# Kernel optimization log

Measured on AMD Instinct MI355X. Metric: run time of the kernel, lower is better.

Reference implementation:

```python
import jax, jax.numpy as jnp
import numpy as np
import math

N_HEAD = 16
DEG = 2
EPS = 1e-7


def setup_inputs() -> dict:
    key = jax.random.key(0)
    k1, k2 = jax.random.split(key)
    B, T, C = 2, 2048, 1024
    x = jax.random.normal(k1, (B, T, C), dtype=jnp.float32)
    W = jax.random.normal(k2, (3 * C + N_HEAD, C), dtype=jnp.float32) * (1.0 / math.sqrt(C))
    return {"x": x, "W": W}


def reference(x, W):
    # JacobAttentionLayer.forward with attention_kernel='powerref' (AttentionReference,
    # deg=2, scale=1/sqrt(hs), eps=1e-7, log-space power softmax, gating=True).
    B, T, C = x.shape
    nh = N_HEAD
    hs = C // nh
    scale = 1.0 / math.sqrt(hs)

    qkvgr = jnp.einsum('btc,oc->bto', x, W)  # [B,T,3C+nh]
    q, k, v = (qkvgr[..., :C], qkvgr[..., C:2 * C], qkvgr[..., 2 * C:3 * C])
    log_g = jax.nn.log_sigmoid(qkvgr[..., 3 * C:].astype(jnp.float32))  # [B,T,nh]
    log_G = jnp.cumsum(log_g, axis=1).transpose(0, 2, 1)  # [B,nh,T]

    def heads(a):  # [B,T,C] -> [B,nh,T,hs]
        return a.reshape(B, T, nh, hs).transpose(0, 2, 1, 3)

    Q, K, V = heads(q), heads(k), heads(v)

    S = jnp.einsum('bhtd,bhsd->bhts', Q, K)  # [B,nh,T,T]
    # log-space power attention: deg*log(|S|+eps) + log(scale) + gating
    Tm = DEG * jnp.log(jnp.abs(S) + EPS) + jnp.log(jnp.float32(scale))
    Z = Tm + log_G[..., :, None] - log_G[..., None, :]
    mask = jnp.tril(jnp.ones((T, T), dtype=bool))
    Z = jnp.where(mask, Z, -jnp.inf)
    Z_rowmax = jax.lax.stop_gradient(jnp.max(Z, axis=-1, keepdims=True))
    P = jnp.exp(Z - Z_rowmax)  # deg even -> no sign correction

    norm = jnp.sum(P, axis=-1)  # [B,nh,T]
    O = jnp.einsum('bhts,bhsd->bhtd', P, V)
    y = O / norm[..., None]
    return y.transpose(0, 2, 1, 3).reshape(B, T, C)
```

## Files before the change

### kernel.cpp

```cpp
#include <hip/hip_runtime.h>
#include <math.h>

typedef __attribute__((ext_vector_type(4))) float f32x4;
typedef __attribute__((ext_vector_type(8))) short short8;

#define NEG_INF (-__builtin_inff())

__device__ __forceinline__ unsigned short f2bf(float f) {
    union { float f; unsigned u; } v; v.f = f;
    unsigned r = v.u + 0x7FFFu + ((v.u >> 16) & 1u);
    return (unsigned short)(r >> 16);
}
__device__ __forceinline__ float bf2f(unsigned short h) {
    union { unsigned u; float f; } v; v.u = ((unsigned)h) << 16;
    return v.f;
}

__device__ __forceinline__ f32x4 mfma_bf16(short8 a, short8 b, f32x4 c) {
    return __builtin_amdgcn_mfma_f32_16x16x32_bf16(a, b, c, 0, 0, 0);
}

__device__ __forceinline__ void gload_lds16(const unsigned short* g, unsigned short* l) {
    __builtin_amdgcn_global_load_lds(
        (const __attribute__((address_space(1))) void*)g,
        (__attribute__((address_space(3))) void*)l, 16, 0, 0);
}

__global__ void split_kernel(const float* __restrict__ in,
                             unsigned short* __restrict__ hi,
                             unsigned short* __restrict__ lo, int n4)
{
    int i = blockIdx.x * 256 + threadIdx.x;
    if (i >= n4) return;
    float4 v = ((const float4*)in)[i];
    ushort4 h, l;
    h.x = f2bf(v.x); l.x = f2bf(v.x - bf2f(h.x));
    h.y = f2bf(v.y); l.y = f2bf(v.y - bf2f(h.y));
    h.z = f2bf(v.z); l.z = f2bf(v.z - bf2f(h.z));
    h.w = f2bf(v.w); l.w = f2bf(v.w - bf2f(h.w));
    ((ushort4*)hi)[i] = h;
    ((ushort4*)lo)[i] = l;
}

__global__ __launch_bounds__(256, 2)
void gemm_proj(const unsigned short* __restrict__ xh, const unsigned short* __restrict__ xl,
               const unsigned short* __restrict__ wh, const unsigned short* __restrict__ wl,
               unsigned short* __restrict__ Qh, unsigned short* __restrict__ Ql,
               unsigned short* __restrict__ Kh, unsigned short* __restrict__ Kl,
               unsigned short* __restrict__ Vtg, float* __restrict__ gbuf)
{
    __shared__ __align__(16) unsigned short Ah[2][128][32];
    __shared__ __align__(16) unsigned short Al[2][128][32];
    __shared__ __align__(16) unsigned short Bh[2][128][32];
    __shared__ __align__(16) unsigned short Bl[2][128][32];

    const int mt = blockIdx.x & 31;
    const int nt = blockIdx.x >> 5;
    const int m0 = mt * 128, n0 = nt * 128;
    const int tid = threadIdx.x;
    const int w = tid >> 6, l = tid & 63;
    const int wm = w >> 1, wn = w & 1;
    const int lr = l & 15, lq = l >> 4;
    const int xs = (lr >> 1) & 3;
    const bool needLo = (nt < 16) || (nt == 24);

    f32x4 acc[4][4];
#pragma unroll
    for (int i = 0; i < 4; ++i)
#pragma unroll
        for (int j = 0; j < 4; ++j) acc[i][j] = (f32x4){0.f, 0.f, 0.f, 0.f};

    const int srow = tid >> 2;
    const int sp = tid & 3;

    auto STAGE = [&](int bsel, int k0) {
#pragma unroll
        for (int p = 0; p < 2; ++p) {
            int r = srow + p * 64;
            int sc = (sp ^ ((r >> 1) & 3)) * 8;
            int o = n0 + r;
            int oc = o < 3088 ? o : 3087;
            gload_lds16(&xh[(size_t)(m0 + r) * 1024 + k0 + sc], &Ah[bsel][r][sp * 8]);
            gload_lds16(&wh[(size_t)oc * 1024 + k0 + sc],       &Bh[bsel][r][sp * 8]);
            if (needLo) {
                gload_lds16(&xl[(size_t)(m0 + r) * 1024 + k0 + sc], &Al[bsel][r][sp * 8]);
                gload_lds16(&wl[(size_t)oc * 1024 + k0 + sc],       &Bl[bsel][r][sp * 8]);
            }
        }
    };

    STAGE(0, 0);
    __asm__ volatile("s_waitcnt vmcnt(0)" ::: "memory");
    __syncthreads();

    int cur = 0;
    for (int k0 = 0; k0 < 1024; k0 += 32) {
        if (k0 + 32 < 1024) STAGE(cur ^ 1, k0 + 32);

        short8 ah[4], bh4[4], al4[4], bl4[4];
#pragma unroll
        for (int i = 0; i < 4; ++i) {
            ah[i]  = *(const short8*)&Ah[cur][wm * 64 + i * 16 + lr][(lq ^ xs) * 8];
            bh4[i] = *(const short8*)&Bh[cur][wn * 64 + i * 16 + lr][(lq ^ xs) * 8];
        }
        if (needLo) {
#pragma unroll
            for (int i = 0; i < 4; ++i) {
                al4[i] = *(const short8*)&Al[cur][wm * 64 + i * 16 + lr][(lq ^ xs) * 8];
                bl4[i] = *(const short8*)&Bl[cur][wn * 64 + i * 16 + lr][(lq ^ xs) * 8];
            }
        }
#pragma unroll
        for (int i = 0; i < 4; ++i)
#pragma unroll
            for (int j = 0; j < 4; ++j) {
                acc[i][j] = mfma_bf16(ah[i], bh4[j], acc[i][j]);
                if (needLo) {
                    acc[i][j] = mfma_bf16(ah[i], bl4[j], acc[i][j]);
                    acc[i][j] = mfma_bf16(al4[i], bh4[j], acc[i][j]);
                }
            }

        __asm__ volatile("s_waitcnt vmcnt(0)" ::: "memory");
        __syncthreads();
        cur ^= 1;
    }

#pragma unroll
    for (int i = 0; i < 4; ++i) {
        int nrow0 = m0 + wm * 64 + i * 16 + lq * 4;
        int b = nrow0 >> 11;
        int tbase = nrow0 & 2047;
#pragma unroll
        for (int j = 0; j < 4; ++j) {
            int o = n0 + wn * 64 + j * 16 + lr;
            if (o < 1024) {
                int h = o >> 6, d = o & 63;
                size_t base = ((size_t)(b * 16 + h) * 2048 + tbase) * 64 + d;
#pragma unroll
                for (int r = 0; r < 4; ++r) {
                    float v = acc[i][j][r];
                    unsigned short hi_ = f2bf(v);
                    unsigned short lo_ = f2bf(v - bf2f(hi_));
                    Qh[base + (size_t)r * 64] = hi_;
                    Ql[base + (size_t)r * 64] = lo_;
                }
            } else if (o < 2048) {
                int oo = o - 1024;
                int h = oo >> 6, d = oo & 63;
                size_t base = ((size_t)(b * 16 + h) * 2048 + tbase) * 64 + d;
#pragma unroll
                for (int r = 0; r < 4; ++r) {
                    float v = acc[i][j][r];
                    unsigned short hi_ = f2bf(v);
                    unsigned short lo_ = f2bf(v - bf2f(hi_));
                    Kh[base + (size_t)r * 64] = hi_;
                    Kl[base + (size_t)r * 64] = lo_;
                }
            } else if (o < 3072) {
                int oo = o - 2048;
                int h = oo >> 6, d = oo & 63;
                size_t base = ((size_t)(b * 16 + h) * 64 + d) * 2048 + tbase;
                ushort4 pk;
                pk.x = f2bf(acc[i][j][0]);
                pk.y = f2bf(acc[i][j][1]);
                pk.z = f2bf(acc[i][j][2]);
                pk.w = f2bf(acc[i][j][3]);
                *(ushort4*)&Vtg[base] = pk;
            } else if (o < 3088) {
                int og = o - 3072;
#pragma unroll
                for (int r = 0; r < 4; ++r)
                    gbuf[(size_t)(nrow0 + r) * 16 + og] = acc[i][j][r];
            }
        }
    }
}

__global__ void gate_scan(const float* __restrict__ g, float* __restrict__ lg)
{
    const int bh = blockIdx.x;
    const int b = bh >> 4, h = bh & 15;
    const int tid = threadIdx.x;
    __shared__ float part[256];

    float vals[8];
    float run = 0.f;
#pragma unroll
    for (int j = 0; j < 8; ++j) {
        int t = tid * 8 + j;
        float x = g[(size_t)(b * 2048 + t) * 16 + h];
        float ls = fminf(x, 0.f) - log1pf(__expf(-fabsf(x)));
        run += ls * 1.4426950408889634f;
        vals[j] = run;
    }
    part[tid] = run;
    __syncthreads();
    for (int ofs = 1; ofs < 256; ofs <<= 1) {
        float add = (tid >= ofs) ? part[tid - ofs] : 0.f;
        __syncthreads();
        part[tid] += add;
        __syncthreads();
    }
    float excl = part[tid] - run;
#pragma unroll
    for (int j = 0; j < 8; ++j)
        lg[(size_t)bh * 2048 + tid * 8 + j] = excl + vals[j];
}

__global__ __launch_bounds__(256, 2)
void attn_fwd(const unsigned short* __restrict__ Qh, const unsigned short* __restrict__ Ql,
              const unsigned short* __restrict__ Kh, const unsigned short* __restrict__ Kl,
              const unsigned short* __restrict__ Vtg, const float* __restrict__ lg,
              float* __restrict__ out)
{
    __shared__ __align__(16) unsigned short kh[2][64][64];
    __shared__ __align__(16) unsigned short kl[2][64][64];
    __shared__ __align__(16) unsigned short vs[2][64][64];
    __shared__ __align__(16) unsigned short pl[4][16][64];

    const int bid = blockIdx.x;
    const int qi = (bid & 7) | ((bid >> 8) << 3);
    const int bh = (bid >> 3) & 31;
    const int tid = threadIdx.x;
    const int w = tid >> 6, l = tid & 63;
    const int lr = l & 15, lq = l >> 4;
    const int xk = lr & 7;
    const int q0 = qi * 64;
    const int myrow0 = q0 + w * 16;

    const size_t qoff = ((size_t)bh * 2048 + myrow0 + lr) * 64;
    short8 qh8[2], ql8[2];
    qh8[0] = *(const short8*)&Qh[qoff + lq * 8];
    qh8[1] = *(const short8*)&Qh[qoff + 32 + lq * 8];
    ql8[0] = *(const short8*)&Ql[qoff + lq * 8];
    ql8[1] = *(const short8*)&Ql[qoff + 32 + lq * 8];

    float gq2[4];
#pragma unroll
    for (int r = 0; r < 4; ++r)
        gq2[r] = lg[(size_t)bh * 2048 + myrow0 + lq * 4 + r] - 3.0f;

    float M_[4]  = {0.f, 0.f, 0.f, 0.f};
    float ls_[4] = {0.f, 0.f, 0.f, 0.f};
    f32x4 o4[4];
#pragma unroll
    for (int i = 0; i < 4; ++i) o4[i] = (f32x4){0.f, 0.f, 0.f, 0.f};

    const int srow = tid >> 3;
    const int schunk = tid & 7;

    const unsigned short* Kh_b = Kh + (size_t)bh * 2048 * 64;
    const unsigned short* Kl_b = Kl + (size_t)bh * 2048 * 64;
    const unsigned short* Vt_b = Vtg + (size_t)bh * 64 * 2048;

    auto STAGE = [&](int bsel, int kv0) {
#pragma unroll
        for (int p = 0; p < 2; ++p) {
            int r = srow + p * 32;
            int sc = (schunk ^ (r & 7)) * 8;
            gload_lds16(&Kh_b[(size_t)(kv0 + r) * 64 + sc], &kh[bsel][r][schunk * 8]);
            gload_lds16(&Kl_b[(size_t)(kv0 + r) * 64 + sc], &kl[bsel][r][schunk * 8]);
            gload_lds16(&Vt_b[(size_t)r * 2048 + kv0 + sc], &vs[bsel][r][schunk * 8]);
        }
    };

    STAGE(0, 0);
    __asm__ volatile("s_waitcnt vmcnt(0)" ::: "memory");
    __syncthreads();

    int cur = 0;
    for (int kv0 = 0; kv0 <= q0; kv0 += 64) {
        if (kv0 + 64 <= q0) STAGE(cur ^ 1, kv0 + 64);

        float gsl[4];
#pragma unroll
        for (int js = 0; js < 4; ++js)
            gsl[js] = lg[(size_t)bh * 2048 + kv0 + js * 16 + lr];

        f32x4 sa[4];
#pragma unroll
        for (int js = 0; js < 4; ++js) sa[js] = (f32x4){0.f, 0.f, 0.f, 0.f};
#pragma unroll
        for (int js = 0; js < 4; ++js)
#pragma unroll
            for (int ks = 0; ks < 2; ++ks) {
                short8 kb  = *(const short8*)&kh[cur][js * 16 + lr][((ks * 4 + lq) ^ xk) << 3];
                short8 kbl = *(const short8*)&kl[cur][js * 16 + lr][((ks * 4 + lq) ^ xk) << 3];
                sa[js] = mfma_bf16(qh8[ks], kb,  sa[js]);
                sa[js] = mfma_bf16(qh8[ks], kbl, sa[js]);
                sa[js] = mfma_bf16(ql8[ks], kb,  sa[js]);
            }

        const bool diag = (kv0 == q0);
#pragma unroll
        for (int js = 0; js < 4; ++js) {
            float ga = gsl[js];
#pragma unroll
            for (int r = 0; r < 4; ++r) {
                float a = fabsf(sa[js][r]) + 1e-7f;
                float ex = exp2f(gq2[r] - ga);
                float wv = a * a * ex;
                if (diag && (js * 16 + lr > w * 16 + lq * 4 + r)) wv = 0.f;
                sa[js][r] = wv;
            }
        }

        float f_[4], rMv[4];
#pragma unroll
        for (int r = 0; r < 4; ++r) {
            float a = fmaxf(fmaxf(sa[0][r], sa[1][r]), fmaxf(sa[2][r], sa[3][r]));
#pragma unroll
            for (int msk = 1; msk < 16; msk <<= 1)
                a = fmaxf(a, __shfl_xor(a, msk, 16));
            float Mn = fmaxf(M_[r], a);
            bool pos = Mn > 1e-30f;
            float rM = pos ? __builtin_amdgcn_rcpf(Mn) : 0.f;
            f_[r]  = pos ? M_[r] * rM : 1.f;
            rMv[r] = rM;
            M_[r]  = Mn;
        }

        float rs_[4] = {0.f, 0.f, 0.f, 0.f};
#pragma unroll
        for (int js = 0; js < 4; ++js)
#pragma unroll
            for (int r = 0; r < 4; ++r) {
                float pv = sa[js][r] * rMv[r];
                sa[js][r] = pv;
                rs_[r] += pv;
            }
#pragma unroll
        for (int r = 0; r < 4; ++r) {
            float s = rs_[r];
#pragma unroll
            for (int msk = 1; msk < 16; msk <<= 1)
                s += __shfl_xor(s, msk, 16);
            ls_[r] = ls_[r] * f_[r] + s;
        }
#pragma unroll
        for (int ds_ = 0; ds_ < 4; ++ds_)
#pragma unroll
            for (int r = 0; r < 4; ++r)
                o4[ds_][r] *= f_[r];

#pragma unroll
        for (int js = 0; js < 4; ++js)
#pragma unroll
            for (int r = 0; r < 4; ++r) {
                int prow = lq * 4 + r;
                int cch = (js * 2 + (lr >> 3)) ^ (prow & 7);
                pl[w][prow][(cch << 3) | (lr & 7)] = f2bf(sa[js][r]);
            }
        __asm__ volatile("s_waitcnt lgkmcnt(0)" ::: "memory");
        __builtin_amdgcn_sched_barrier(0);

        short8 pa0 = *(const short8*)&pl[w][lr][((0 + lq) ^ xk) << 3];
        short8 pa1 = *(const short8*)&pl[w][lr][((4 + lq) ^ xk) << 3];
#pragma unroll
        for (int ds_ = 0; ds_ < 4; ++ds_) {
            short8 vb0 = *(const short8*)&vs[cur][ds_ * 16 + lr][((0 + lq) ^ xk) << 3];
            short8 vb1 = *(const short8*)&vs[cur][ds_ * 16 + lr][((4 + lq) ^ xk) << 3];
            o4[ds_] = mfma_bf16(pa0, vb0, o4[ds_]);
            o4[ds_] = mfma_bf16(pa1, vb1, o4[ds_]);
        }

        __asm__ volatile("s_waitcnt vmcnt(0)" ::: "memory");
        __syncthreads();
        cur ^= 1;
    }

    const int b = bh >> 4, h = bh & 15;
#pragma unroll
    for (int ds_ = 0; ds_ < 4; ++ds_)
#pragma unroll
        for (int r = 0; r < 4; ++r) {
            int t = myrow0 + lq * 4 + r;
            out[(size_t)(b * 2048 + t) * 1024 + h * 64 + ds_ * 16 + lr] =
                o4[ds_][r] / ls_[r];
        }
}

extern "C" void kernel_launch(void* const* d_in, const int* in_sizes, int n_in,
                              void* d_out, int out_size, void* d_ws, size_t ws_size,
                              hipStream_t stream)
{
    const float* x = (const float*)d_in[0];
    const float* W = (const float*)d_in[1];
    float* out = (float*)d_out;

    const size_t NX = 4194304;
    const size_t NW = 3162112;
    const size_t NQ = 4194304;

    char* ws = (char*)d_ws;
    size_t off = 0;
    auto alloc = [&](size_t bytes) -> void* {
        void* p = ws + off;
        off += (bytes + 255) & ~(size_t)255;
        return p;
    };
    unsigned short* xh = (unsigned short*)alloc(NX * 2);
    unsigned short* xl = (unsigned short*)alloc(NX * 2);
    unsigned short* wh = (unsigned short*)alloc(NW * 2);
    unsigned short* wl = (unsigned short*)alloc(NW * 2);
    unsigned short* Qh = (unsigned short*)alloc(NQ * 2);
    unsigned short* Ql = (unsigned short*)alloc(NQ * 2);
    unsigned short* Kh = (unsigned short*)alloc(NQ * 2);
    unsigned short* Kl = (unsigned short*)alloc(NQ * 2);
    unsigned short* Vt = (unsigned short*)alloc(NQ * 2);
    float* g  = (float*)alloc(65536 * 4);
    float* lg = (float*)alloc(65536 * 4);
    if (off > ws_size) return;

    split_kernel<<<(int)(NX / 4 + 255) / 256, 256, 0, stream>>>(x, xh, xl, (int)(NX / 4));
    split_kernel<<<(int)(NW / 4 + 255) / 256, 256, 0, stream>>>(W, wh, wl, (int)(NW / 4));
    gemm_proj<<<800, 256, 0, stream>>>(xh, xl, wh, wl, Qh, Ql, Kh, Kl, Vt, g);
    gate_scan<<<32, 256, 0, stream>>>(g, lg);
    attn_fwd<<<1024, 256, 0, stream>>>(Qh, Ql, Kh, Kl, Vt, lg, out);
}
```

Baseline: 222.8 us.

## Single-buffer KV tiles, raise occupancy, and pair causal q-tiles in block ordering

Drops the double-buffered K/V LDS staging in favour of a single buffer that is loaded and waited on at the start of each iteration, and raises launch bounds to three blocks per CU. This reduces LDS use per block so more blocks can be resident and hide latency through occupancy rather than prefetch. It also remaps block IDs so consecutive blocks alternate short and long causal q-tiles, to balance the triangular workload across the grid. The cost is that global-to-LDS loads are no longer overlapped with compute within a block, and the tighter register budget may cause spills.

New measurement: 208.5 us. 6.4% less time.

```diff
diff --git a/kernel.cpp b/kernel.cpp
--- a/kernel.cpp
+++ b/kernel.cpp
@@ -208,20 +208,23 @@
         lg[(size_t)bh * 2048 + tid * 8 + j] = excl + vals[j];
 }
 
-__global__ __launch_bounds__(256, 2)
+__global__ __launch_bounds__(256, 3)
 void attn_fwd(const unsigned short* __restrict__ Qh, const unsigned short* __restrict__ Ql,
               const unsigned short* __restrict__ Kh, const unsigned short* __restrict__ Kl,
               const unsigned short* __restrict__ Vtg, const float* __restrict__ lg,
               float* __restrict__ out)
 {
-    __shared__ __align__(16) unsigned short kh[2][64][64];
-    __shared__ __align__(16) unsigned short kl[2][64][64];
-    __shared__ __align__(16) unsigned short vs[2][64][64];
+    __shared__ __align__(16) unsigned short kh[64][64];
+    __shared__ __align__(16) unsigned short kl[64][64];
+    __shared__ __align__(16) unsigned short vs[64][64];
     __shared__ __align__(16) unsigned short pl[4][16][64];
 
     const int bid = blockIdx.x;
-    const int qi = (bid & 7) | ((bid >> 8) << 3);
-    const int bh = (bid >> 3) & 31;
+    const int x8 = bid & 7;
+    const int k  = bid >> 3;
+    const int m  = k >> 2;
+    const int bh = x8 + 8 * (k & 3);
+    const int qi = (m & 1) ? (31 - (m >> 1)) : (m >> 1);
     const int tid = threadIdx.x;
     const int w = tid >> 6, l = tid & 63;
     const int lr = l & 15, lq = l >> 4;
@@ -254,24 +257,18 @@
     const unsigned short* Kl_b = Kl + (size_t)bh * 2048 * 64;
     const unsigned short* Vt_b = Vtg + (size_t)bh * 64 * 2048;
 
-    auto STAGE = [&](int bsel, int kv0) {
+    for (int kv0 = 0; kv0 <= q0; kv0 += 64) {
+        __syncthreads();
 #pragma unroll
         for (int p = 0; p < 2; ++p) {
             int r = srow + p * 32;
             int sc = (schunk ^ (r & 7)) * 8;
-            gload_lds16(&Kh_b[(size_t)(kv0 + r) * 64 + sc], &kh[bsel][r][schunk * 8]);
-            gload_lds16(&Kl_b[(size_t)(kv0 + r) * 64 + sc], &kl[bsel][r][schunk * 8]);
-            gload_lds16(&Vt_b[(size_t)r * 2048 + kv0 + sc], &vs[bsel][r][schunk * 8]);
-        }
-    };
-
-    STAGE(0, 0);
-    __asm__ volatile("s_waitcnt vmcnt(0)" ::: "memory");
-    __syncthreads();
-
-    int cur = 0;
-    for (int kv0 = 0; kv0 <= q0; kv0 += 64) {
-        if (kv0 + 64 <= q0) STAGE(cur ^ 1, kv0 + 64);
+            gload_lds16(&Kh_b[(size_t)(kv0 + r) * 64 + sc], &kh[r][schunk * 8]);
+            gload_lds16(&Kl_b[(size_t)(kv0 + r) * 64 + sc], &kl[r][schunk * 8]);
+            gload_lds16(&Vt_b[(size_t)r * 2048 + kv0 + sc], &vs[r][schunk * 8]);
+        }
+        __asm__ volatile("s_waitcnt vmcnt(0)" ::: "memory");
+        __syncthreads();
 
         float gsl[4];
 #pragma unroll
@@ -285,8 +282,8 @@
         for (int js = 0; js < 4; ++js)
 #pragma unroll
             for (int ks = 0; ks < 2; ++ks) {
-                short8 kb  = *(const short8*)&kh[cur][js * 16 + lr][((ks * 4 + lq) ^ xk) << 3];
-                short8 kbl = *(const short8*)&kl[cur][js * 16 + lr][((ks * 4 + lq) ^ xk) << 3];
+                short8 kb  = *(const short8*)&kh[js * 16 + lr][((ks * 4 + lq) ^ xk) << 3];
+                short8 kbl = *(const short8*)&kl[js * 16 + lr][((ks * 4 + lq) ^ xk) << 3];
                 sa[js] = mfma_bf16(qh8[ks], kb,  sa[js]);
                 sa[js] = mfma_bf16(qh8[ks], kbl, sa[js]);
                 sa[js] = mfma_bf16(ql8[ks], kb,  sa[js]);
@@ -359,15 +356,11 @@
         short8 pa1 = *(const short8*)&pl[w][lr][((4 + lq) ^ xk) << 3];
 #pragma unroll
         for (int ds_ = 0; ds_ < 4; ++ds_) {
-            short8 vb0 = *(const short8*)&vs[cur][ds_ * 16 + lr][((0 + lq) ^ xk) << 3];
-            short8 vb1 = *(const short8*)&vs[cur][ds_ * 16 + lr][((4 + lq) ^ xk) << 3];
+            short8 vb0 = *(const short8*)&vs[ds_ * 16 + lr][((0 + lq) ^ xk) << 3];
+            short8 vb1 = *(const short8*)&vs[ds_ * 16 + lr][((4 + lq) ^ xk) << 3];
             o4[ds_] = mfma_bf16(pa0, vb0, o4[ds_]);
             o4[ds_] = mfma_bf16(pa1, vb1, o4[ds_]);
         }
-
-        __asm__ volatile("s_waitcnt vmcnt(0)" ::: "memory");
-        __syncthreads();
-        cur ^= 1;
     }
 
     const int b = bh >> 4, h = bh & 15;
```
